# Kernel optimization log

Measured on AMD Instinct MI355X. Metric: run time of the kernel, lower is better.

## Reference

```python
import jax, jax.numpy as jnp
import numpy as np

N_S, N_T, E = 50000, 50000, 600000
D_IN, D_H, D_OUT = 256, 128, 64


def setup_inputs() -> dict:
    key = jax.random.key(0)
    k1, k2, k3, k4, k5, k6 = jax.random.split(key, 6)
    edge_src = jax.random.randint(k1, (E,), 0, N_S, dtype=jnp.int32)
    edge_dst = jax.random.randint(k2, (E,), 0, N_T, dtype=jnp.int32)
    edge_index = jnp.stack([edge_src, edge_dst], axis=0)  # [2, E]
    x_s = jax.random.normal(k3, (N_S, D_IN), dtype=jnp.float32)
    x_t = jax.random.normal(k4, (N_T, D_IN), dtype=jnp.float32)
    W0 = jax.random.normal(k5, (D_IN, D_H), dtype=jnp.float32) * (1.0 / np.sqrt(D_IN))
    W1 = jax.random.normal(k6, (D_H, D_OUT), dtype=jnp.float32) * (1.0 / np.sqrt(D_H))
    return {"edge_index": edge_index, "x_s": x_s, "x_t": x_t, "W0": W0, "W1": W1}


def gcn_conv(x, src, dst, W):
    """PyG GCNConv, bias=False: D^{-1/2}(A+I)D^{-1/2} (x @ W)."""
    N = x.shape[0]
    h = x @ W  # [N, out]
    loops = jnp.arange(N, dtype=src.dtype)
    s = jnp.concatenate([src, loops])  # add self-loops
    d = jnp.concatenate([dst, loops])
    deg = jax.ops.segment_sum(jnp.ones_like(d, dtype=h.dtype), d, num_segments=N)
    dinv = jnp.where(deg > 0, jax.lax.rsqrt(deg), 0.0)
    norm = dinv[s] * dinv[d]  # [E+N]
    return jax.ops.segment_sum(h[s] * norm[:, None], d, num_segments=N)


def reference(edge_index, x_s, x_t, W0, W1):
    n_s = x_s.shape[0]
    src = edge_index[0]
    dst = edge_index[1] + n_s  # targets live in the x_t block
    acts = [jax.nn.relu, lambda v: v]
    Ws = [W0, W1]
    for W, act in zip(Ws, acts):
        x = jnp.concatenate([x_s, x_t], axis=0)
        x = act(gcn_conv(x, src, dst, W))
        x_s, x_t = x[:n_s], x[n_s:]
    return (x_s, x_t)
```

## Files before the change

kernel.cpp:

```cpp
#include <hip/hip_runtime.h>
#include <cstdint>
#include <cstddef>

typedef unsigned short u16;
typedef unsigned int   u32;
typedef __attribute__((ext_vector_type(8))) short bf16x8;
typedef __attribute__((ext_vector_type(4))) float f32x4;

#define D_IN  256
#define D_H   128
#define D_OUT 64

__device__ __forceinline__ float bf2f(u16 u){
  union { u32 i; float f; } v; v.i = ((u32)u) << 16; return v.f;
}
__device__ __forceinline__ u16 f2bf(float f){
  union { float f; u32 i; } v; v.f = f;
  u32 r = (v.i + 0x7fffu + ((v.i >> 16) & 1u)) >> 16;
  return (u16)r;
}

__global__ void k_wprep(const float* __restrict__ W0, const float* __restrict__ W1,
                        u16* __restrict__ W0t, u16* __restrict__ W1t,
                        int* __restrict__ deg, int n_t){
  int i = blockIdx.x * 256 + threadIdx.x;
  if (i < 128 * 256){
    int n = i >> 8, k = i & 255;
    W0t[i] = f2bf(W0[(size_t)k * 128 + n]);
  } else if (i < 128 * 256 + 64 * 128){
    int j = i - 128 * 256;
    int n = j >> 7, k = j & 127;
    W1t[j] = f2bf(W1[(size_t)k * 64 + n]);
  } else if (i - (128 * 256 + 64 * 128) < n_t){
    deg[i - (128 * 256 + 64 * 128)] = 0;
  }
}

__global__ void k_deg(const int* __restrict__ dst, int E, int* __restrict__ deg){
  int e = blockIdx.x * 256 + threadIdx.x;
  if (e < E) atomicAdd(&deg[dst[e]], 1);
}

__global__ __launch_bounds__(256) void k_bsum(const int* __restrict__ deg, int N,
                                              int* __restrict__ bsum){
  __shared__ int s[256];
  int tid = threadIdx.x;
  int i = blockIdx.x * 256 + tid;
  s[tid] = (i < N) ? deg[i] : 0;
  __syncthreads();
  for (int o = 128; o > 0; o >>= 1){
    if (tid < o) s[tid] += s[tid + o];
    __syncthreads();
  }
  if (tid == 0) bsum[blockIdx.x] = s[0];
}

__global__ __launch_bounds__(256) void k_off(const int* __restrict__ deg, int N,
                                             const int* __restrict__ bsum, int nb,
                                             int* __restrict__ off, int* __restrict__ cursor,
                                             float* __restrict__ dinv){
  __shared__ int s[256];
  __shared__ int sbase[256];
  const int tid = threadIdx.x;
  const int bid = blockIdx.x;
  const int i   = bid * 256 + tid;
  int acc = 0;
  for (int j = tid; j < bid; j += 256) acc += bsum[j];
  sbase[tid] = acc;
  int v = (i < N) ? deg[i] : 0;
  s[tid] = v;
  __syncthreads();
  for (int o = 128; o > 0; o >>= 1){
    if (tid < o) sbase[tid] += sbase[tid + o];
    __syncthreads();
  }
  for (int o = 1; o < 256; o <<= 1){
    int t = (tid >= o) ? s[tid - o] : 0;
    __syncthreads();
    s[tid] += t;
    __syncthreads();
  }
  if (i < N){
    int excl = s[tid] - v + sbase[0];
    off[i] = excl;
    cursor[i] = excl;
    dinv[i] = rsqrtf((float)v + 1.0f);
  }
}

__global__ void k_fill(const int* __restrict__ src, const int* __restrict__ dst,
                       int E, int* __restrict__ cursor, int* __restrict__ csr){
  int e = blockIdx.x * 256 + threadIdx.x;
  if (e < E){
    int d = dst[e];
    int p = atomicAdd(&cursor[d], 1);
    csr[p] = src[e];
  }
}

__global__ __launch_bounds__(512, 4) void k_gemm1(
    const float* __restrict__ Xs, const float* __restrict__ Xt,
    const u16* __restrict__ W0t, int M, int n_s,
    u16* __restrict__ out)
{
  __shared__ u16 Bs[128 * 256];
  const int t    = threadIdx.x;
  const int wave = t >> 6, lane = t & 63;
  const int lm   = lane & 15, quad = lane >> 4;
  const int gw   = blockIdx.x * 8 + wave;
  const int row  = gw * 16 + lm;

  int cr = (row < M) ? row : 0;
  const float* pa = ((cr < n_s) ? (Xs + (size_t)cr * D_IN)
                                : (Xt + (size_t)(cr - n_s) * D_IN)) + quad * 8;

  float4 a[8][2];
  a[0][0] = *(const float4*)(pa +  0); a[0][1] = *(const float4*)(pa +  4);
  a[1][0] = *(const float4*)(pa + 32); a[1][1] = *(const float4*)(pa + 36);

  {
    const int n = t >> 2;
    const int c = t & 3;
    const u16* wsrc = W0t + (size_t)n * 256 + c * 64;
    char* brow = (char*)Bs + n * 512;
    const int sw = (n & 15) << 4;
    #pragma unroll
    for (int j = 0; j < 8; j++){
      int off = (c * 128 + j * 16) ^ sw;
      *(int4*)(brow + off) = *(const int4*)(wsrc + j * 8);
    }
  }

  #pragma unroll
  for (int s = 2; s < 8; s++){
    a[s][0] = *(const float4*)(pa + s * 32);
    a[s][1] = *(const float4*)(pa + s * 32 + 4);
  }

  f32x4 acc[8];
  const f32x4 z = {0.f, 0.f, 0.f, 0.f};
  #pragma unroll
  for (int nf = 0; nf < 8; nf++) acc[nf] = z;

  __syncthreads();

  const char* bb = (const char*)Bs + lm * 512;
  const int lmx = lm << 4;

  #pragma unroll
  for (int kk = 0; kk < 8; kk++){
    bf16x8 af;
    {
      const float* fa = (const float*)&a[kk][0];
      u16 tmp[8];
      #pragma unroll
      for (int q = 0; q < 8; q++) tmp[q] = f2bf(fa[q]);
      af = *(const bf16x8*)tmp;
    }
    const int koff = (kk * 64 + quad * 16) ^ lmx;
    #pragma unroll
    for (int nf = 0; nf < 8; nf++){
      bf16x8 bf = *(const bf16x8*)(bb + nf * 8192 + koff);
      acc[nf] = __builtin_amdgcn_mfma_f32_16x16x32_bf16(af, bf, acc[nf], 0, 0, 0);
    }
  }

  {
    int rbase = gw * 16 + quad * 4;
    #pragma unroll
    for (int rr = 0; rr < 4; rr++){
      int m = rbase + rr;
      if (m >= M) continue;
      u16* op = out + (size_t)m * D_H + lm;
      #pragma unroll
      for (int nf = 0; nf < 8; nf++)
        op[nf * 16] = f2bf(acc[nf][rr]);
    }
  }
}

__global__ __launch_bounds__(256) void k_aggf(
    const int* __restrict__ off, const int* __restrict__ deg,
    const int* __restrict__ csr, const float* __restrict__ dinv,
    u16* __restrict__ h1, int n_s, int n_t)
{
  int w    = (blockIdx.x * 256 + threadIdx.x) >> 6;
  int lane = threadIdx.x & 63;
  if (w >= n_t) return;
  const int g = lane >> 4;
  const int c = lane & 15;
  int start = off[w];
  int n     = deg[w];

  float r[8], p[8];
  #pragma unroll
  for (int q = 0; q < 8; q++){ r[q] = 0.f; p[q] = 0.f; }

  int i = 0;
  for (; i + 8 <= n; i += 8){
    int sa = csr[start + i + g];
    int sb = csr[start + i + 4 + g];
    int4 da = *(const int4*)(h1 + (size_t)sa * D_H + c * 8);
    int4 db = *(const int4*)(h1 + (size_t)sb * D_H + c * 8);
    const u16* ha = (const u16*)&da;
    const u16* hb = (const u16*)&db;
    #pragma unroll
    for (int q = 0; q < 8; q++){
      float va = bf2f(ha[q]), vb = bf2f(hb[q]);
      r[q] += va + vb;
      p[q] += fmaxf(va, 0.f) + fmaxf(vb, 0.f);
    }
  }
  for (; i < n; i += 4){
    if (i + g < n){
      int sa = csr[start + i + g];
      int4 da = *(const int4*)(h1 + (size_t)sa * D_H + c * 8);
      const u16* ha = (const u16*)&da;
      #pragma unroll
      for (int q = 0; q < 8; q++){
        float va = bf2f(ha[q]);
        r[q] += va;
        p[q] += fmaxf(va, 0.f);
      }
    }
  }

  #pragma unroll
  for (int q = 0; q < 8; q++){
    r[q] += __shfl_xor(r[q], 16, 64);
    r[q] += __shfl_xor(r[q], 32, 64);
    p[q] += __shfl_xor(p[q], 16, 64);
    p[q] += __shfl_xor(p[q], 32, 64);
  }

  if (g == 0){
    float di  = dinv[w];
    float di2 = di * di;
    u16* selfp = h1 + (size_t)(n_s + w) * D_H + c * 8;
    int4 hs = *(const int4*)selfp;
    const u16* hh = (const u16*)&hs;
    u16 ob[8];
    #pragma unroll
    for (int q = 0; q < 8; q++){
      float zq = fmaxf(di * r[q] + di2 * bf2f(hh[q]), 0.f);
      float uq = di * p[q] + di2 * zq;
      ob[q] = f2bf(uq);
    }
    *(int4*)selfp = *(int4*)ob;
  }
}

__device__ __forceinline__ bf16x8 relu_bf(int4 v, bool relu){
  const u16* s = (const u16*)&v;
  u16 tmp[8];
  #pragma unroll
  for (int q = 0; q < 8; q++){
    u16 x = s[q];
    tmp[q] = (relu && (x & 0x8000u)) ? (u16)0 : x;
  }
  return *(const bf16x8*)tmp;
}

__global__ __launch_bounds__(512, 4) void k_gemm2(
    const u16* __restrict__ h1, const u16* __restrict__ W1t,
    int M, int n_s, float* __restrict__ out)
{
  __shared__ u16 Bs[64 * 128];
  const int t    = threadIdx.x;
  const int wave = t >> 6, lane = t & 63;
  const int lm   = lane & 15, quad = lane >> 4;
  const int gw   = blockIdx.x * 8 + wave;
  const int row  = gw * 16 + lm;

  int cr = (row < M) ? row : 0;
  const bool relu = (row < n_s);
  const u16* pa = h1 + (size_t)cr * D_H + quad * 8;

  int4 a[4];
  a[0] = *(const int4*)(pa);
  a[1] = *(const int4*)(pa + 32);

  {
    const int n = t >> 3;
    const int c = t & 7;
    const u16* wsrc = W1t + (size_t)n * 128 + c * 16;
    char* brow = (char*)Bs + n * 256;
    const int sw = (n & 15) << 4;
    #pragma unroll
    for (int j = 0; j < 2; j++){
      int off = (c * 32 + j * 16) ^ sw;
      *(int4*)(brow + off) = *(const int4*)(wsrc + j * 8);
    }
  }
  a[2] = *(const int4*)(pa + 64);
  a[3] = *(const int4*)(pa + 96);

  f32x4 acc[4];
  const f32x4 z = {0.f, 0.f, 0.f, 0.f};
  #pragma unroll
  for (int nf = 0; nf < 4; nf++) acc[nf] = z;

  __syncthreads();

  const char* bb = (const char*)Bs + lm * 256;
  const int lmx = lm << 4;

  #pragma unroll
  for (int kk = 0; kk < 4; kk++){
    bf16x8 af = relu_bf(a[kk], relu);
    const int koff = (kk * 64 + quad * 16) ^ lmx;
    #pragma unroll
    for (int nf = 0; nf < 4; nf++){
      bf16x8 bf = *(const bf16x8*)(bb + nf * 4096 + koff);
      acc[nf] = __builtin_amdgcn_mfma_f32_16x16x32_bf16(af, bf, acc[nf], 0, 0, 0);
    }
  }

  {
    int rbase = gw * 16 + quad * 4;
    #pragma unroll
    for (int rr = 0; rr < 4; rr++){
      int m = rbase + rr;
      if (m >= M) continue;
      float* op = out + (size_t)m * D_OUT + lm;
      #pragma unroll
      for (int nf = 0; nf < 4; nf++)
        op[nf * 16] = acc[nf][rr];
    }
  }
}

static inline size_t alup(size_t x){ return (x + 255) & ~(size_t)255; }

extern "C" void kernel_launch(void* const* d_in, const int* in_sizes, int n_in,
                              void* d_out, int out_size, void* d_ws, size_t ws_size,
                              hipStream_t stream)
{
  const int*   ei = (const int*)d_in[0];
  const float* xs = (const float*)d_in[1];
  const float* xt = (const float*)d_in[2];
  const float* W0 = (const float*)d_in[3];
  const float* W1 = (const float*)d_in[4];
  const int E   = in_sizes[0] / 2;
  const int n_s = in_sizes[1] / D_IN;
  const int n_t = in_sizes[2] / D_IN;
  const int M   = n_s + n_t;
  const int* src = ei;
  const int* dst = ei + E;
  const int nb_t = (n_t + 255) / 256;

  char* p = (char*)d_ws;
  int*   deg    = (int*)p;    p += alup((size_t)n_t * 4);
  int*   off    = (int*)p;    p += alup((size_t)n_t * 4);
  int*   cursor = (int*)p;    p += alup((size_t)n_t * 4);
  float* dinv   = (float*)p;  p += alup((size_t)n_t * 4);
  int*   bsum   = (int*)p;    p += alup((size_t)nb_t * 4);
  int*   csr    = (int*)p;    p += alup((size_t)E * 4);
  u16*   W0t    = (u16*)p;    p += alup((size_t)D_H * D_IN * 2);
  u16*   W1t    = (u16*)p;    p += alup((size_t)D_OUT * D_H * 2);
  u16*   h1     = (u16*)p;    p += alup((size_t)M * D_H * 2);

  const int wprep_n = 128*256 + 64*128 + n_t;
  k_wprep <<<(wprep_n + 255) / 256, 256, 0, stream>>>(W0, W1, W0t, W1t, deg, n_t);
  k_deg   <<<(E + 255) / 256, 256, 0, stream>>>(dst, E, deg);
  k_bsum  <<<nb_t, 256, 0, stream>>>(deg, n_t, bsum);
  k_off   <<<nb_t, 256, 0, stream>>>(deg, n_t, bsum, nb_t, off, cursor, dinv);
  k_fill  <<<(E + 255) / 256, 256, 0, stream>>>(src, dst, E, cursor, csr);

  k_gemm1<<<(M + 127) / 128, 512, 0, stream>>>(xs, xt, W0t, M, n_s, h1);
  k_aggf <<<(n_t + 3) / 4, 256, 0, stream>>>(off, deg, csr, dinv, h1, n_s, n_t);
  k_gemm2<<<(M + 127) / 128, 512, 0, stream>>>(h1, W1t, M, n_s, (float*)d_out);
}
```

Baseline: 255.6 us.

## Fuse degree counting into GEMM1, merge aggregation with source-side GEMM2

Folds the degree atomics into the first GEMM kernel and drops the block-sum kernel, so the offset kernel re-sums the prefix of deg directly. The aggregation kernel and the source-row half of the second GEMM now share one launch, since source rows do not depend on the aggregation. The target-row half of GEMM2 runs in a separate kernel afterward. This cuts launch count and overlaps independent work, at the cost of a quadratic-ish prefix re-read in k_off and extra atomics inside the GEMM kernel.

Measured after the change: 270.1 us. 1.06x slower.

```diff
diff --git a/kernel.cpp b/kernel.cpp
--- a/kernel.cpp
+++ b/kernel.cpp
@@ -36,27 +36,7 @@
   }
 }
 
-__global__ void k_deg(const int* __restrict__ dst, int E, int* __restrict__ deg){
-  int e = blockIdx.x * 256 + threadIdx.x;
-  if (e < E) atomicAdd(&deg[dst[e]], 1);
-}
-
-__global__ __launch_bounds__(256) void k_bsum(const int* __restrict__ deg, int N,
-                                              int* __restrict__ bsum){
-  __shared__ int s[256];
-  int tid = threadIdx.x;
-  int i = blockIdx.x * 256 + tid;
-  s[tid] = (i < N) ? deg[i] : 0;
-  __syncthreads();
-  for (int o = 128; o > 0; o >>= 1){
-    if (tid < o) s[tid] += s[tid + o];
-    __syncthreads();
-  }
-  if (tid == 0) bsum[blockIdx.x] = s[0];
-}
-
 __global__ __launch_bounds__(256) void k_off(const int* __restrict__ deg, int N,
-                                             const int* __restrict__ bsum, int nb,
                                              int* __restrict__ off, int* __restrict__ cursor,
                                              float* __restrict__ dinv){
   __shared__ int s[256];
@@ -65,7 +45,8 @@
   const int bid = blockIdx.x;
   const int i   = bid * 256 + tid;
   int acc = 0;
-  for (int j = tid; j < bid; j += 256) acc += bsum[j];
+  const int lim = bid * 256;
+  for (int j = tid; j < lim; j += 256) acc += deg[j];
   sbase[tid] = acc;
   int v = (i < N) ? deg[i] : 0;
   s[tid] = v;
@@ -75,9 +56,9 @@
     __syncthreads();
   }
   for (int o = 1; o < 256; o <<= 1){
-    int t = (tid >= o) ? s[tid - o] : 0;
+    int tv = (tid >= o) ? s[tid - o] : 0;
     __syncthreads();
-    s[tid] += t;
+    s[tid] += tv;
     __syncthreads();
   }
   if (i < N){
@@ -98,9 +79,10 @@
   }
 }
 
-__global__ __launch_bounds__(512, 4) void k_gemm1(
+__global__ __launch_bounds__(512, 4) void k_g1deg(
     const float* __restrict__ Xs, const float* __restrict__ Xt,
     const u16* __restrict__ W0t, int M, int n_s,
+    const int* __restrict__ dst, int E, int* __restrict__ deg,
     u16* __restrict__ out)
 {
   __shared__ u16 Bs[128 * 256];
@@ -119,6 +101,15 @@
   a[1][0] = *(const float4*)(pa + 32); a[1][1] = *(const float4*)(pa + 36);
 
   {
+    const int stride = (int)gridDim.x * 512;
+    int e = blockIdx.x * 512 + t;
+    if (e < E) atomicAdd(&deg[dst[e]], 1);
+    e += stride;
+    if (e < E) atomicAdd(&deg[dst[e]], 1);
+    for (e += stride; e < E; e += stride) atomicAdd(&deg[dst[e]], 1);
+  }
+
+  {
     const int n = t >> 2;
     const int c = t & 3;
     const u16* wsrc = W0t + (size_t)n * 256 + c * 64;
@@ -136,6 +127,7 @@
     a[s][0] = *(const float4*)(pa + s * 32);
     a[s][1] = *(const float4*)(pa + s * 32 + 4);
   }
+  __builtin_amdgcn_sched_barrier(0);
 
   f32x4 acc[8];
   const f32x4 z = {0.f, 0.f, 0.f, 0.f};
@@ -179,13 +171,11 @@
   }
 }
 
-__global__ __launch_bounds__(256) void k_aggf(
+__device__ __forceinline__ void aggf_body(
     const int* __restrict__ off, const int* __restrict__ deg,
     const int* __restrict__ csr, const float* __restrict__ dinv,
-    u16* __restrict__ h1, int n_s, int n_t)
-{
-  int w    = (blockIdx.x * 256 + threadIdx.x) >> 6;
-  int lane = threadIdx.x & 63;
+    u16* __restrict__ h1, int n_s, int n_t, int w, int lane)
+{
   if (w >= n_t) return;
   const int g = lane >> 4;
   const int c = lane & 15;
@@ -261,19 +251,19 @@
   return *(const bf16x8*)tmp;
 }
 
-__global__ __launch_bounds__(512, 4) void k_gemm2(
+__device__ __forceinline__ void gemm2_body(
     const u16* __restrict__ h1, const u16* __restrict__ W1t,
-    int M, int n_s, float* __restrict__ out)
-{
-  __shared__ u16 Bs[64 * 128];
+    int gb, int base, int rowLim, int n_s, float* __restrict__ out,
+    u16* Bs)
+{
   const int t    = threadIdx.x;
   const int wave = t >> 6, lane = t & 63;
   const int lm   = lane & 15, quad = lane >> 4;
-  const int gw   = blockIdx.x * 8 + wave;
-  const int row  = gw * 16 + lm;
-
-  int cr = (row < M) ? row : 0;
-  const bool relu = (row < n_s);
+  const int gw   = gb * 8 + wave;
+  const int row  = base + gw * 16 + lm;
+
+  int cr = (row < rowLim) ? row : base;
+  const bool relu = (cr < n_s);
   const u16* pa = h1 + (size_t)cr * D_H + quad * 8;
 
   int4 a[4];
@@ -294,6 +284,7 @@
   }
   a[2] = *(const int4*)(pa + 64);
   a[3] = *(const int4*)(pa + 96);
+  __builtin_amdgcn_sched_barrier(0);
 
   f32x4 acc[4];
   const f32x4 z = {0.f, 0.f, 0.f, 0.f};
@@ -317,17 +308,40 @@
   }
 
   {
-    int rbase = gw * 16 + quad * 4;
+    int rbase = base + gw * 16 + quad * 4;
     #pragma unroll
     for (int rr = 0; rr < 4; rr++){
       int m = rbase + rr;
-      if (m >= M) continue;
+      if (m >= rowLim) continue;
       float* op = out + (size_t)m * D_OUT + lm;
       #pragma unroll
       for (int nf = 0; nf < 4; nf++)
         op[nf * 16] = acc[nf][rr];
     }
   }
+}
+
+__global__ __launch_bounds__(512, 4) void k_agg2s(
+    const int* __restrict__ off, const int* __restrict__ deg,
+    const int* __restrict__ csr, const float* __restrict__ dinv,
+    u16* __restrict__ h1, int n_s, int n_t,
+    const u16* __restrict__ W1t, float* __restrict__ out, int nbAgg)
+{
+  __shared__ u16 Bs[64 * 128];
+  if ((int)blockIdx.x < nbAgg){
+    int w = blockIdx.x * 8 + (threadIdx.x >> 6);
+    aggf_body(off, deg, csr, dinv, h1, n_s, n_t, w, threadIdx.x & 63);
+  } else {
+    gemm2_body(h1, W1t, (int)blockIdx.x - nbAgg, 0, n_s, n_s, out, Bs);
+  }
+}
+
+__global__ __launch_bounds__(512, 4) void k_g2t(
+    const u16* __restrict__ h1, const u16* __restrict__ W1t,
+    int M, int n_s, float* __restrict__ out)
+{
+  __shared__ u16 Bs[64 * 128];
+  gemm2_body(h1, W1t, (int)blockIdx.x, n_s, M, n_s, out, Bs);
 }
 
 static inline size_t alup(size_t x){ return (x + 255) & ~(size_t)255; }
@@ -347,27 +361,29 @@
   const int M   = n_s + n_t;
   const int* src = ei;
   const int* dst = ei + E;
-  const int nb_t = (n_t + 255) / 256;
 
   char* p = (char*)d_ws;
   int*   deg    = (int*)p;    p += alup((size_t)n_t * 4);
   int*   off    = (int*)p;    p += alup((size_t)n_t * 4);
   int*   cursor = (int*)p;    p += alup((size_t)n_t * 4);
   float* dinv   = (float*)p;  p += alup((size_t)n_t * 4);
-  int*   bsum   = (int*)p;    p += alup((size_t)nb_t * 4);
   int*   csr    = (int*)p;    p += alup((size_t)E * 4);
   u16*   W0t    = (u16*)p;    p += alup((size_t)D_H * D_IN * 2);
   u16*   W1t    = (u16*)p;    p += alup((size_t)D_OUT * D_H * 2);
   u16*   h1     = (u16*)p;    p += alup((size_t)M * D_H * 2);
 
+  const int nb_t   = (n_t + 255) / 256;
+  const int nbG1   = (M + 127) / 128;
+  const int nbAgg  = (n_t + 7) / 8;
+  const int nbG2s  = (n_s + 127) / 128;
+  const int nbG2t  = (n_t + 127) / 128;
+
   const int wprep_n = 128*256 + 64*128 + n_t;
   k_wprep <<<(wprep_n + 255) / 256, 256, 0, stream>>>(W0, W1, W0t, W1t, deg, n_t);
-  k_deg   <<<(E + 255) / 256, 256, 0, stream>>>(dst, E, deg);
-  k_bsum  <<<nb_t, 256, 0, stream>>>(deg, n_t, bsum);
-  k_off   <<<nb_t, 256, 0, stream>>>(deg, n_t, bsum, nb_t, off, cursor, dinv);
+  k_g1deg <<<nbG1, 512, 0, stream>>>(xs, xt, W0t, M, n_s, dst, E, deg, h1);
+  k_off   <<<nb_t, 256, 0, stream>>>(deg, n_t, off, cursor, dinv);
   k_fill  <<<(E + 255) / 256, 256, 0, stream>>>(src, dst, E, cursor, csr);
-
-  k_gemm1<<<(M + 127) / 128, 512, 0, stream>>>(xs, xt, W0t, M, n_s, h1);
-  k_aggf <<<(n_t + 3) / 4, 256, 0, stream>>>(off, deg, csr, dinv, h1, n_s, n_t);
-  k_gemm2<<<(M + 127) / 128, 512, 0, stream>>>(h1, W1t, M, n_s, (float*)d_out);
-}
+  k_agg2s <<<nbAgg + nbG2s, 512, 0, stream>>>(off, deg, csr, dinv, h1, n_s, n_t,
+                                              W1t, (float*)d_out, nbAgg);
+  k_g2t   <<<nbG2t, 512, 0, stream>>>(h1, W1t, M, n_s, (float*)d_out);
+}
```
